# Kernel optimization log

Hardware: AMD Instinct MI355X
Metric: run time of the kernel (lower is better)

## Reference

```python
import jax, jax.numpy as jnp
import numpy as np

BN_EPS = 1e-5
LN_EPS = 1e-5


def setup_inputs() -> dict:
    key = jax.random.key(0)
    ks = jax.random.split(key, 8)
    B, D, T = 16, 96, 512  # batch, enc_in (channels), d_model (time/feature)
    H = 2 * T
    residual = jax.random.normal(ks[0], (B, D, T), dtype=jnp.float32)
    # BatchNorm1d(enc_in) affine params
    bn_gamma = jnp.ones((D,), dtype=jnp.float32)
    bn_beta = jnp.zeros((D,), dtype=jnp.float32)
    # LayerNorm(d_model) affine params
    ln_gamma = jnp.ones((T,), dtype=jnp.float32)
    ln_beta = jnp.zeros((T,), dtype=jnp.float32)
    # MLP: Linear(T, 2T) -> GELU -> Linear(2T, T)
    W1 = jax.random.normal(ks[1], (T, H), dtype=jnp.float32) / np.float32(np.sqrt(T))
    b1 = jnp.zeros((H,), dtype=jnp.float32)
    W2 = jax.random.normal(ks[2], (H, T), dtype=jnp.float32) / np.float32(np.sqrt(H))
    b2 = jnp.zeros((T,), dtype=jnp.float32)
    return {"residual": residual, "bn_gamma": bn_gamma, "bn_beta": bn_beta,
            "ln_gamma": ln_gamma, "ln_beta": ln_beta,
            "W1": W1, "b1": b1, "W2": W2, "b2": b2}


def _var_cor_attention(x):
    # x: [B, D, T]; queries = keys = values = x
    B, D, T = x.shape
    f = jnp.fft.rfft(x, axis=-1)                       # [B, D, F]
    # pairwise spectral product q_i * conj(k_j): [B, D, D, F]
    res = f[:, :, None, :] * jnp.conj(f[:, None, :, :])
    corr = jnp.fft.irfft(res, axis=-1).mean(axis=-1)   # [B, D, D]
    scale = np.float32(1.0 / np.sqrt(T))
    corr = jax.nn.softmax(corr * scale, axis=-1)
    V = jnp.einsum('bsd,bde->bse', corr, x)            # [B, D, T]
    return V


def reference(residual, bn_gamma, bn_beta, ln_gamma, ln_beta, W1, b1, W2, b2):
    # attention + residual
    x = _var_cor_attention(residual) + residual        # [B, D, T]
    # BatchNorm1d over channel dim D: stats over (B, T), biased variance
    mu = x.mean(axis=(0, 2), keepdims=True)
    var = ((x - mu) ** 2).mean(axis=(0, 2), keepdims=True)
    x = (x - mu) * jax.lax.rsqrt(var + BN_EPS)
    x = x * bn_gamma[None, :, None] + bn_beta[None, :, None]
    # MLP (exact GELU, torch default) + residual
    h = jax.nn.gelu(jnp.einsum('bdt,th->bdh', x, W1) + b1, approximate=False)
    y = jnp.einsum('bdh,ht->bdt', h, W2) + b2 + x
    # LayerNorm over last dim T
    mu2 = y.mean(axis=-1, keepdims=True)
    var2 = ((y - mu2) ** 2).mean(axis=-1, keepdims=True)
    y = (y - mu2) * jax.lax.rsqrt(var2 + LN_EPS)
    return y * ln_gamma + ln_beta
```

## Files before the change

kernel.cpp:

```cpp
#include <hip/hip_runtime.h>
#include <math.h>
#include <stdint.h>

#define BB 16
#define DD 96
#define TT 512
#define HH 1024
#define NROW (BB*DD)

typedef __attribute__((ext_vector_type(4))) float floatx4;
typedef __attribute__((ext_vector_type(8))) short short8;

#define WSOFF_X     0
#define WSOFF_HFRAG 0
#define WSOFF_XROW  (3*1024*1024)
#define WSOFF_XFRAG (WSOFF_XROW + NROW*TT*2)
#define WSOFF_W1BF  (WSOFF_XFRAG + NROW*TT*2)
#define WSOFF_W2BF  (WSOFF_W1BF + TT*HH*2)
#define WSOFF_A     (WSOFF_W2BF + HH*TT*2)
#define WSOFF_P1    (WSOFF_A + BB*DD*DD*4)
#define WSOFF_P2    (WSOFF_P1 + DD*128*4)

__device__ __forceinline__ uint16_t f2bf(float v) {
    uint32_t u = __float_as_uint(v);
    uint32_t r = 0x7fffu + ((u >> 16) & 1u);
    return (uint16_t)((u + r) >> 16);
}
__device__ __forceinline__ float bf2f(uint16_t v) {
    return __uint_as_float(((uint32_t)v) << 16);
}

#define KT1 (TT/32)
#define KT2 (HH/32)
__device__ __forceinline__ size_t afrag1_slot(int row, int k) {
    return ((size_t)((row >> 4)*KT1 + (k >> 5))*64 + ((k >> 3) & 3)*16 + (row & 15));
}

__global__ __launch_bounds__(256) void k_prep(const float* __restrict__ r,
                                              float* __restrict__ A) {
    __shared__ float sl[DD];
    int b = blockIdx.x;
    int tid = threadIdx.x;
    int w = tid >> 6, lane = tid & 63;
    for (int rr = 0; rr < 24; ++rr) {
        int i = w*24 + rr;
        const float* p = r + ((size_t)b*DD + i)*TT;
        float acc = 0.f;
        #pragma unroll
        for (int s = 0; s < TT/64; ++s) acc += p[lane + s*64];
        #pragma unroll
        for (int o = 32; o > 0; o >>= 1) acc += __shfl_down(acc, o, 64);
        if (lane == 0) sl[i] = acc;
    }
    __syncthreads();
    int i = tid;
    if (i < DD) {
        const float c = 1.0f / (512.0f * 22.627416997969522f);
        float si = sl[i] * c;
        float m = -1e30f;
        for (int j = 0; j < DD; ++j) m = fmaxf(m, si * sl[j]);
        float sum = 0.f;
        for (int j = 0; j < DD; ++j) sum += expf(si * sl[j] - m);
        float inv = 1.0f / sum;
        float* Ao = A + ((size_t)b*DD + i)*DD;
        for (int j = 0; j < DD; ++j) Ao[j] = expf(si * sl[j] - m) * inv;
    }
}

__global__ __launch_bounds__(256) void k_attw(const float* __restrict__ r,
                                              const float* __restrict__ A,
                                              const float* __restrict__ W1,
                                              const float* __restrict__ W2,
                                              float* __restrict__ x,
                                              uint16_t* __restrict__ w1bf,
                                              uint16_t* __restrict__ w2bf,
                                              float* __restrict__ P1,
                                              float* __restrict__ P2) {
    int bx = blockIdx.x;
    int tid = threadIdx.x;
    int w = tid >> 6, lane = tid & 63;
    if (bx < 512) {
        int blk = bx*4 + w;
        int q = lane >> 4, l15 = lane & 15;
        const float* W; uint16_t* out; int KT, N, b;
        if (blk < 1024) { W = W1; out = w1bf; KT = 16; N = 1024; b = blk; }
        else            { W = W2; out = w2bf; KT = 32; N = 512;  b = blk - 1024; }
        int tile_n = b / KT, tile_k = b % KT;
        const float* src = W + (size_t)(tile_k*32 + q*8)*N + tile_n*16 + l15;
        uint16_t tmp[8];
        #pragma unroll
        for (int j = 0; j < 8; ++j) tmp[j] = f2bf(src[(size_t)j*N]);
        uint16_t* dst = out + ((size_t)b*64 + lane)*8;
        *reinterpret_cast<ushort4*>(dst)     = *reinterpret_cast<ushort4*>(&tmp[0]);
        *reinterpret_cast<ushort4*>(dst + 4) = *reinterpret_cast<ushort4*>(&tmp[4]);
        return;
    }
    __shared__ float rlds[DD*64];
    int idx = bx - 512;
    int b = idx & 15, chunk = (idx >> 4) & 7, ig = idx >> 7;
    int t0 = chunk * 64;
    const float4* rb4 = reinterpret_cast<const float4*>(r + (size_t)b*DD*TT);
    float4* rl4 = reinterpret_cast<float4*>(rlds);
    #pragma unroll
    for (int s = 0; s < 6; ++s) {
        int ii = tid + s*256;
        rl4[ii] = rb4[(size_t)(ii >> 4)*(TT/4) + (t0 >> 2) + (ii & 15)];
    }
    __syncthreads();
    int wu = __builtin_amdgcn_readfirstlane(w);
    int i0 = ig*24 + wu*6;
    const float* Ab = A + ((size_t)b*DD + i0)*DD;
    float acc[6];
    #pragma unroll
    for (int rr = 0; rr < 6; ++rr) acc[rr] = rlds[(i0+rr)*64 + lane];
    #pragma unroll 4
    for (int j4 = 0; j4 < DD/4; ++j4) {
        float4 a[6];
        #pragma unroll
        for (int rr = 0; rr < 6; ++rr)
            a[rr] = *reinterpret_cast<const float4*>(Ab + rr*DD + j4*4);
        float rv[4];
        #pragma unroll
        for (int u = 0; u < 4; ++u) rv[u] = rlds[(j4*4+u)*64 + lane];
        #pragma unroll
        for (int rr = 0; rr < 6; ++rr) {
            acc[rr] = fmaf(a[rr].x, rv[0], acc[rr]);
            acc[rr] = fmaf(a[rr].y, rv[1], acc[rr]);
            acc[rr] = fmaf(a[rr].z, rv[2], acc[rr]);
            acc[rr] = fmaf(a[rr].w, rv[3], acc[rr]);
        }
    }
    int p = b*8 + chunk;
    #pragma unroll
    for (int rr = 0; rr < 6; ++rr) {
        int i = i0 + rr;
        x[((size_t)b*DD + i)*TT + t0 + lane] = acc[rr];
        float ls = acc[rr], ls2 = acc[rr]*acc[rr];
        #pragma unroll
        for (int o = 32; o > 0; o >>= 1) {
            ls  += __shfl_down(ls,  o, 64);
            ls2 += __shfl_down(ls2, o, 64);
        }
        if (lane == 0) { P1[i*128 + p] = ls; P2[i*128 + p] = ls2; }
    }
}

__global__ __launch_bounds__(256) void k_bnx(const float* __restrict__ x,
                                             const float* __restrict__ P1,
                                             const float* __restrict__ P2,
                                             const float* __restrict__ g,
                                             const float* __restrict__ bt,
                                             uint16_t* __restrict__ xrow,
                                             uint16_t* __restrict__ xfrag) {
    __shared__ float rr1[4], rr2[4], scsh[4];
    int blk = blockIdx.x;
    int tid = threadIdx.x;
    int wid = tid >> 6, lane = tid & 63;
    int r0 = blk*2;
    int d0 = r0 % DD, d1 = (r0+1) % DD;
    int d = (wid < 2) ? d0 : d1;
    int p = (wid & 1)*64 + lane;
    float v1 = P1[d*128 + p], v2 = P2[d*128 + p];
    #pragma unroll
    for (int o = 32; o > 0; o >>= 1) {
        v1 += __shfl_down(v1, o, 64);
        v2 += __shfl_down(v2, o, 64);
    }
    if (lane == 0) { rr1[wid] = v1; rr2[wid] = v2; }
    __syncthreads();
    if (tid < 2) {
        float s1 = rr1[tid*2] + rr1[tid*2+1];
        float s2 = rr2[tid*2] + rr2[tid*2+1];
        const float invn = 1.0f / (float)(BB*TT);
        float mu  = s1 * invn;
        float var = s2 * invn - mu*mu;
        float rs  = rsqrtf(var + 1e-5f);
        int dd = (tid == 0) ? d0 : d1;
        float scale = rs * g[dd];
        scsh[tid*2]   = scale;
        scsh[tid*2+1] = bt[dd] - mu*scale;
    }
    __syncthreads();
    int half = tid >> 7;
    int row = r0 + half;
    int k0 = (tid & 127) * 4;
    float scd = scsh[half*2], shd = scsh[half*2+1];
    float4 v = *reinterpret_cast<const float4*>(&x[(size_t)row*TT + k0]);
    ushort4 o;
    o.x = f2bf(v.x*scd + shd);
    o.y = f2bf(v.y*scd + shd);
    o.z = f2bf(v.z*scd + shd);
    o.w = f2bf(v.w*scd + shd);
    *reinterpret_cast<ushort4*>(&xrow[(size_t)row*TT + k0]) = o;
    size_t slot = afrag1_slot(row, k0);
    *reinterpret_cast<ushort4*>(&xfrag[slot*8 + (k0 & 7)]) = o;
}

__global__ __launch_bounds__(256) void k_gemm1(const uint16_t* __restrict__ xfrag,
                                               const uint16_t* __restrict__ w1bf,
                                               const float* __restrict__ b1,
                                               uint16_t* __restrict__ hfrag) {
    __shared__ __align__(16) uint16_t cs[16][136];
    int tid = threadIdx.x;
    int wave = tid >> 6, lane = tid & 63;
    int q = lane >> 4, l15 = lane & 15;
    int mtile = blockIdx.x;
    int n0 = blockIdx.y * 128 + wave * 32;
    floatx4 acc[2] = {};
    const uint16_t* ap  = xfrag + ((size_t)mtile*KT1*64 + lane)*8;
    const uint16_t* b0p = w1bf + ((size_t)((n0>>4)    )*16*64 + lane)*8;
    const uint16_t* b1p = w1bf + ((size_t)((n0>>4) + 1)*16*64 + lane)*8;
    #pragma unroll
    for (int kk = 0; kk < 16; ++kk) {
        short8 a  = *reinterpret_cast<const short8*>(ap  + kk*512);
        short8 b0 = *reinterpret_cast<const short8*>(b0p + kk*512);
        short8 b1 = *reinterpret_cast<const short8*>(b1p + kk*512);
        acc[0] = __builtin_amdgcn_mfma_f32_16x16x32_bf16(a, b0, acc[0], 0, 0, 0);
        acc[1] = __builtin_amdgcn_mfma_f32_16x16x32_bf16(a, b1, acc[1], 0, 0, 0);
    }
    #pragma unroll
    for (int nf = 0; nf < 2; ++nf) {
        int coll = wave*32 + nf*16 + l15;
        float bias = b1[blockIdx.y*128 + coll];
        #pragma unroll
        for (int r = 0; r < 4; ++r) {
            float v = acc[nf][r] + bias;
            float gl = 0.5f * v * (1.0f + erff(v * 0.7071067811865475f));
            cs[q*4 + r][coll] = f2bf(gl);
        }
    }
    __syncthreads();
    int c = wave;
    const uint4* src = reinterpret_cast<const uint4*>(&cs[l15][c*32 + q*8]);
    size_t chunk = (size_t)mtile*KT2 + (blockIdx.y*4 + c);
    reinterpret_cast<uint4*>(hfrag)[chunk*64 + lane] = *src;
}

__global__ __launch_bounds__(256) void k_gemm2(const uint16_t* __restrict__ hfrag,
                                               const uint16_t* __restrict__ w2bf,
                                               const float* __restrict__ b2,
                                               const uint16_t* __restrict__ xrow,
                                               float* __restrict__ y) {
    int tid = threadIdx.x;
    int wave = tid >> 6, lane = tid & 63;
    int q = lane >> 4, l15 = lane & 15;
    int mtile = blockIdx.x;
    int m0 = mtile * 16;
    int n0 = blockIdx.y * 128 + wave * 32;
    floatx4 acc[2] = {};
    const uint16_t* ap  = hfrag + ((size_t)mtile*KT2*64 + lane)*8;
    const uint16_t* b0p = w2bf + ((size_t)((n0>>4)    )*32*64 + lane)*8;
    const uint16_t* b1p = w2bf + ((size_t)((n0>>4) + 1)*32*64 + lane)*8;
    #pragma unroll
    for (int kk = 0; kk < 32; ++kk) {
        short8 a  = *reinterpret_cast<const short8*>(ap  + kk*512);
        short8 b0 = *reinterpret_cast<const short8*>(b0p + kk*512);
        short8 b1 = *reinterpret_cast<const short8*>(b1p + kk*512);
        acc[0] = __builtin_amdgcn_mfma_f32_16x16x32_bf16(a, b0, acc[0], 0, 0, 0);
        acc[1] = __builtin_amdgcn_mfma_f32_16x16x32_bf16(a, b1, acc[1], 0, 0, 0);
    }
    #pragma unroll
    for (int nf = 0; nf < 2; ++nf) {
        int col = n0 + nf*16 + l15;
        float bias = b2[col];
        #pragma unroll
        for (int r = 0; r < 4; ++r) {
            int row = m0 + q*4 + r;
            float xb = bf2f(xrow[(size_t)row*TT + col]);
            y[(size_t)row*TT + col] = acc[nf][r] + bias + xb;
        }
    }
}

__global__ __launch_bounds__(64) void k_ln(float* __restrict__ y,
                                           const float* __restrict__ lng,
                                           const float* __restrict__ lnb) {
    int row = blockIdx.x;
    int lane = threadIdx.x;
    float4* p = reinterpret_cast<float4*>(y + (size_t)row*TT);
    float4 v0 = p[lane*2], v1 = p[lane*2 + 1];
    float s  = v0.x+v0.y+v0.z+v0.w + v1.x+v1.y+v1.z+v1.w;
    float s2 = v0.x*v0.x+v0.y*v0.y+v0.z*v0.z+v0.w*v0.w
             + v1.x*v1.x+v1.y*v1.y+v1.z*v1.z+v1.w*v1.w;
    #pragma unroll
    for (int o = 1; o < 64; o <<= 1) {
        s  += __shfl_xor(s,  o, 64);
        s2 += __shfl_xor(s2, o, 64);
    }
    float mu = s * (1.0f/TT);
    float var = s2 * (1.0f/TT) - mu*mu;
    float rs = rsqrtf(var + 1e-5f);
    const float4* g4 = reinterpret_cast<const float4*>(lng);
    const float4* b4 = reinterpret_cast<const float4*>(lnb);
    float4 g0 = g4[lane*2], g1 = g4[lane*2+1];
    float4 bb0 = b4[lane*2], bb1 = b4[lane*2+1];
    float4 o0, o1;
    o0.x = (v0.x-mu)*rs*g0.x + bb0.x;  o0.y = (v0.y-mu)*rs*g0.y + bb0.y;
    o0.z = (v0.z-mu)*rs*g0.z + bb0.z;  o0.w = (v0.w-mu)*rs*g0.w + bb0.w;
    o1.x = (v1.x-mu)*rs*g1.x + bb1.x;  o1.y = (v1.y-mu)*rs*g1.y + bb1.y;
    o1.z = (v1.z-mu)*rs*g1.z + bb1.z;  o1.w = (v1.w-mu)*rs*g1.w + bb1.w;
    p[lane*2] = o0;  p[lane*2+1] = o1;
}

extern "C" void kernel_launch(void* const* d_in, const int* in_sizes, int n_in,
                              void* d_out, int out_size, void* d_ws, size_t ws_size,
                              hipStream_t stream) {
    (void)in_sizes; (void)n_in; (void)out_size; (void)ws_size;
    const float* residual = (const float*)d_in[0];
    const float* bng = (const float*)d_in[1];
    const float* bnb = (const float*)d_in[2];
    const float* lng = (const float*)d_in[3];
    const float* lnb = (const float*)d_in[4];
    const float* W1  = (const float*)d_in[5];
    const float* b1  = (const float*)d_in[6];
    const float* W2  = (const float*)d_in[7];
    const float* b2  = (const float*)d_in[8];
    float* out = (float*)d_out;
    char* ws = (char*)d_ws;
    float*    x     = (float*)(ws + WSOFF_X);
    uint16_t* hfrag = (uint16_t*)(ws + WSOFF_HFRAG);
    uint16_t* xrow  = (uint16_t*)(ws + WSOFF_XROW);
    uint16_t* xfrag = (uint16_t*)(ws + WSOFF_XFRAG);
    uint16_t* w1bf  = (uint16_t*)(ws + WSOFF_W1BF);
    uint16_t* w2bf  = (uint16_t*)(ws + WSOFF_W2BF);
    float*    A     = (float*)(ws + WSOFF_A);
    float*    P1    = (float*)(ws + WSOFF_P1);
    float*    P2    = (float*)(ws + WSOFF_P2);

    k_prep<<<BB, 256, 0, stream>>>(residual, A);
    k_attw<<<1024, 256, 0, stream>>>(residual, A, W1, W2, x, w1bf, w2bf, P1, P2);
    k_bnx<<<NROW/2, 256, 0, stream>>>(x, P1, P2, bng, bnb, xrow, xfrag);
    k_gemm1<<<dim3(96, 8), 256, 0, stream>>>(xfrag, w1bf, b1, hfrag);
    k_gemm2<<<dim3(96, 4), 256, 0, stream>>>(hfrag, w2bf, b2, xrow, out);
    k_ln<<<NROW, 64, 0, stream>>>(out, lng, lnb);
}
```

Measured before the change: 127.9 us.

## Fuse all stages into one cooperative persistent kernel with grid syncs

Replaces the six separate kernel launches with a single cooperative kernel of 512 blocks that runs each stage in turn, separated by grid-wide barriers. It also parallelises the row sums and softmax of the attention weights across many blocks, where the old prep kernel used only 16 blocks. The aim is to remove launch gaps and the serial prep bottleneck. In exchange it adds grid.sync costs, caps the grid at 512 blocks with stage loops, and falls back to seven ordinary launches if the cooperative launch fails.

```diff
diff --git a/kernel.cpp b/kernel.cpp
--- a/kernel.cpp
+++ b/kernel.cpp
@@ -1,6 +1,9 @@
 #include <hip/hip_runtime.h>
+#include <hip/hip_cooperative_groups.h>
 #include <math.h>
 #include <stdint.h>
+
+namespace cg = cooperative_groups;
 
 #define BB 16
 #define DD 96
@@ -12,7 +15,6 @@
 typedef __attribute__((ext_vector_type(8))) short short8;
 
 #define WSOFF_X     0
-#define WSOFF_HFRAG 0
 #define WSOFF_XROW  (3*1024*1024)
 #define WSOFF_XFRAG (WSOFF_XROW + NROW*TT*2)
 #define WSOFF_W1BF  (WSOFF_XFRAG + NROW*TT*2)
@@ -20,6 +22,7 @@
 #define WSOFF_A     (WSOFF_W2BF + HH*TT*2)
 #define WSOFF_P1    (WSOFF_A + BB*DD*DD*4)
 #define WSOFF_P2    (WSOFF_P1 + DD*128*4)
+#define WSOFF_S     (WSOFF_P2 + DD*128*4)
 
 __device__ __forceinline__ uint16_t f2bf(float v) {
     uint32_t u = __float_as_uint(v);
@@ -36,270 +39,278 @@
     return ((size_t)((row >> 4)*KT1 + (k >> 5))*64 + ((k >> 3) & 3)*16 + (row & 15));
 }
 
-__global__ __launch_bounds__(256) void k_prep(const float* __restrict__ r,
-                                              float* __restrict__ A) {
-    __shared__ float sl[DD];
-    int b = blockIdx.x;
-    int tid = threadIdx.x;
-    int w = tid >> 6, lane = tid & 63;
-    for (int rr = 0; rr < 24; ++rr) {
-        int i = w*24 + rr;
-        const float* p = r + ((size_t)b*DD + i)*TT;
-        float acc = 0.f;
-        #pragma unroll
-        for (int s = 0; s < TT/64; ++s) acc += p[lane + s*64];
-        #pragma unroll
-        for (int o = 32; o > 0; o >>= 1) acc += __shfl_down(acc, o, 64);
-        if (lane == 0) sl[i] = acc;
-    }
-    __syncthreads();
-    int i = tid;
-    if (i < DD) {
-        const float c = 1.0f / (512.0f * 22.627416997969522f);
-        float si = sl[i] * c;
-        float m = -1e30f;
-        for (int j = 0; j < DD; ++j) m = fmaxf(m, si * sl[j]);
-        float sum = 0.f;
-        for (int j = 0; j < DD; ++j) sum += expf(si * sl[j] - m);
-        float inv = 1.0f / sum;
-        float* Ao = A + ((size_t)b*DD + i)*DD;
-        for (int j = 0; j < DD; ++j) Ao[j] = expf(si * sl[j] - m) * inv;
-    }
-}
-
-__global__ __launch_bounds__(256) void k_attw(const float* __restrict__ r,
-                                              const float* __restrict__ A,
-                                              const float* __restrict__ W1,
-                                              const float* __restrict__ W2,
-                                              float* __restrict__ x,
-                                              uint16_t* __restrict__ w1bf,
-                                              uint16_t* __restrict__ w2bf,
-                                              float* __restrict__ P1,
-                                              float* __restrict__ P2) {
+__global__ __launch_bounds__(256, 4) void k_fused(
+        int plo, int phi, int coop,
+        const float* __restrict__ r,
+        const float* __restrict__ bng, const float* __restrict__ bnb,
+        const float* __restrict__ lng, const float* __restrict__ lnb,
+        const float* __restrict__ W1,  const float* __restrict__ b1,
+        const float* __restrict__ W2,  const float* __restrict__ b2,
+        float* __restrict__ out,
+        float* __restrict__ x, uint16_t* __restrict__ xrow,
+        uint16_t* __restrict__ xfrag, uint16_t* __restrict__ w1bf,
+        uint16_t* __restrict__ w2bf, float* __restrict__ A,
+        float* __restrict__ P1, float* __restrict__ P2,
+        float* __restrict__ s) {
+    cg::grid_group grid = cg::this_grid();
+    __shared__ __align__(16) float sbuf[DD*64];
+    uint16_t* hfrag = reinterpret_cast<uint16_t*>(x);
     int bx = blockIdx.x;
     int tid = threadIdx.x;
     int w = tid >> 6, lane = tid & 63;
-    if (bx < 512) {
-        int blk = bx*4 + w;
-        int q = lane >> 4, l15 = lane & 15;
-        const float* W; uint16_t* out; int KT, N, b;
-        if (blk < 1024) { W = W1; out = w1bf; KT = 16; N = 1024; b = blk; }
-        else            { W = W2; out = w2bf; KT = 32; N = 512;  b = blk - 1024; }
-        int tile_n = b / KT, tile_k = b % KT;
-        const float* src = W + (size_t)(tile_k*32 + q*8)*N + tile_n*16 + l15;
-        uint16_t tmp[8];
+    int q = lane >> 4, l15 = lane & 15;
+
+    if (plo <= 0 && 0 <= phi) {
         #pragma unroll
-        for (int j = 0; j < 8; ++j) tmp[j] = f2bf(src[(size_t)j*N]);
-        uint16_t* dst = out + ((size_t)b*64 + lane)*8;
-        *reinterpret_cast<ushort4*>(dst)     = *reinterpret_cast<ushort4*>(&tmp[0]);
-        *reinterpret_cast<ushort4*>(dst + 4) = *reinterpret_cast<ushort4*>(&tmp[4]);
-        return;
-    }
-    __shared__ float rlds[DD*64];
-    int idx = bx - 512;
-    int b = idx & 15, chunk = (idx >> 4) & 7, ig = idx >> 7;
-    int t0 = chunk * 64;
-    const float4* rb4 = reinterpret_cast<const float4*>(r + (size_t)b*DD*TT);
-    float4* rl4 = reinterpret_cast<float4*>(rlds);
-    #pragma unroll
-    for (int s = 0; s < 6; ++s) {
-        int ii = tid + s*256;
-        rl4[ii] = rb4[(size_t)(ii >> 4)*(TT/4) + (t0 >> 2) + (ii & 15)];
-    }
-    __syncthreads();
-    int wu = __builtin_amdgcn_readfirstlane(w);
-    int i0 = ig*24 + wu*6;
-    const float* Ab = A + ((size_t)b*DD + i0)*DD;
-    float acc[6];
-    #pragma unroll
-    for (int rr = 0; rr < 6; ++rr) acc[rr] = rlds[(i0+rr)*64 + lane];
-    #pragma unroll 4
-    for (int j4 = 0; j4 < DD/4; ++j4) {
-        float4 a[6];
-        #pragma unroll
-        for (int rr = 0; rr < 6; ++rr)
-            a[rr] = *reinterpret_cast<const float4*>(Ab + rr*DD + j4*4);
-        float rv[4];
-        #pragma unroll
-        for (int u = 0; u < 4; ++u) rv[u] = rlds[(j4*4+u)*64 + lane];
-        #pragma unroll
-        for (int rr = 0; rr < 6; ++rr) {
-            acc[rr] = fmaf(a[rr].x, rv[0], acc[rr]);
-            acc[rr] = fmaf(a[rr].y, rv[1], acc[rr]);
-            acc[rr] = fmaf(a[rr].z, rv[2], acc[rr]);
-            acc[rr] = fmaf(a[rr].w, rv[3], acc[rr]);
-        }
-    }
-    int p = b*8 + chunk;
-    #pragma unroll
-    for (int rr = 0; rr < 6; ++rr) {
-        int i = i0 + rr;
-        x[((size_t)b*DD + i)*TT + t0 + lane] = acc[rr];
-        float ls = acc[rr], ls2 = acc[rr]*acc[rr];
-        #pragma unroll
-        for (int o = 32; o > 0; o >>= 1) {
-            ls  += __shfl_down(ls,  o, 64);
-            ls2 += __shfl_down(ls2, o, 64);
-        }
-        if (lane == 0) { P1[i*128 + p] = ls; P2[i*128 + p] = ls2; }
-    }
-}
-
-__global__ __launch_bounds__(256) void k_bnx(const float* __restrict__ x,
-                                             const float* __restrict__ P1,
-                                             const float* __restrict__ P2,
-                                             const float* __restrict__ g,
-                                             const float* __restrict__ bt,
-                                             uint16_t* __restrict__ xrow,
-                                             uint16_t* __restrict__ xfrag) {
-    __shared__ float rr1[4], rr2[4], scsh[4];
-    int blk = blockIdx.x;
-    int tid = threadIdx.x;
-    int wid = tid >> 6, lane = tid & 63;
-    int r0 = blk*2;
-    int d0 = r0 % DD, d1 = (r0+1) % DD;
-    int d = (wid < 2) ? d0 : d1;
-    int p = (wid & 1)*64 + lane;
-    float v1 = P1[d*128 + p], v2 = P2[d*128 + p];
-    #pragma unroll
-    for (int o = 32; o > 0; o >>= 1) {
-        v1 += __shfl_down(v1, o, 64);
-        v2 += __shfl_down(v2, o, 64);
-    }
-    if (lane == 0) { rr1[wid] = v1; rr2[wid] = v2; }
-    __syncthreads();
-    if (tid < 2) {
-        float s1 = rr1[tid*2] + rr1[tid*2+1];
-        float s2 = rr2[tid*2] + rr2[tid*2+1];
-        const float invn = 1.0f / (float)(BB*TT);
-        float mu  = s1 * invn;
-        float var = s2 * invn - mu*mu;
-        float rs  = rsqrtf(var + 1e-5f);
-        int dd = (tid == 0) ? d0 : d1;
-        float scale = rs * g[dd];
-        scsh[tid*2]   = scale;
-        scsh[tid*2+1] = bt[dd] - mu*scale;
-    }
-    __syncthreads();
-    int half = tid >> 7;
-    int row = r0 + half;
-    int k0 = (tid & 127) * 4;
-    float scd = scsh[half*2], shd = scsh[half*2+1];
-    float4 v = *reinterpret_cast<const float4*>(&x[(size_t)row*TT + k0]);
-    ushort4 o;
-    o.x = f2bf(v.x*scd + shd);
-    o.y = f2bf(v.y*scd + shd);
-    o.z = f2bf(v.z*scd + shd);
-    o.w = f2bf(v.w*scd + shd);
-    *reinterpret_cast<ushort4*>(&xrow[(size_t)row*TT + k0]) = o;
-    size_t slot = afrag1_slot(row, k0);
-    *reinterpret_cast<ushort4*>(&xfrag[slot*8 + (k0 & 7)]) = o;
-}
-
-__global__ __launch_bounds__(256) void k_gemm1(const uint16_t* __restrict__ xfrag,
-                                               const uint16_t* __restrict__ w1bf,
-                                               const float* __restrict__ b1,
-                                               uint16_t* __restrict__ hfrag) {
-    __shared__ __align__(16) uint16_t cs[16][136];
-    int tid = threadIdx.x;
-    int wave = tid >> 6, lane = tid & 63;
-    int q = lane >> 4, l15 = lane & 15;
-    int mtile = blockIdx.x;
-    int n0 = blockIdx.y * 128 + wave * 32;
-    floatx4 acc[2] = {};
-    const uint16_t* ap  = xfrag + ((size_t)mtile*KT1*64 + lane)*8;
-    const uint16_t* b0p = w1bf + ((size_t)((n0>>4)    )*16*64 + lane)*8;
-    const uint16_t* b1p = w1bf + ((size_t)((n0>>4) + 1)*16*64 + lane)*8;
-    #pragma unroll
-    for (int kk = 0; kk < 16; ++kk) {
-        short8 a  = *reinterpret_cast<const short8*>(ap  + kk*512);
-        short8 b0 = *reinterpret_cast<const short8*>(b0p + kk*512);
-        short8 b1 = *reinterpret_cast<const short8*>(b1p + kk*512);
-        acc[0] = __builtin_amdgcn_mfma_f32_16x16x32_bf16(a, b0, acc[0], 0, 0, 0);
-        acc[1] = __builtin_amdgcn_mfma_f32_16x16x32_bf16(a, b1, acc[1], 0, 0, 0);
-    }
-    #pragma unroll
-    for (int nf = 0; nf < 2; ++nf) {
-        int coll = wave*32 + nf*16 + l15;
-        float bias = b1[blockIdx.y*128 + coll];
-        #pragma unroll
-        for (int r = 0; r < 4; ++r) {
-            float v = acc[nf][r] + bias;
-            float gl = 0.5f * v * (1.0f + erff(v * 0.7071067811865475f));
-            cs[q*4 + r][coll] = f2bf(gl);
-        }
-    }
-    __syncthreads();
-    int c = wave;
-    const uint4* src = reinterpret_cast<const uint4*>(&cs[l15][c*32 + q*8]);
-    size_t chunk = (size_t)mtile*KT2 + (blockIdx.y*4 + c);
-    reinterpret_cast<uint4*>(hfrag)[chunk*64 + lane] = *src;
-}
-
-__global__ __launch_bounds__(256) void k_gemm2(const uint16_t* __restrict__ hfrag,
-                                               const uint16_t* __restrict__ w2bf,
-                                               const float* __restrict__ b2,
-                                               const uint16_t* __restrict__ xrow,
-                                               float* __restrict__ y) {
-    int tid = threadIdx.x;
-    int wave = tid >> 6, lane = tid & 63;
-    int q = lane >> 4, l15 = lane & 15;
-    int mtile = blockIdx.x;
-    int m0 = mtile * 16;
-    int n0 = blockIdx.y * 128 + wave * 32;
-    floatx4 acc[2] = {};
-    const uint16_t* ap  = hfrag + ((size_t)mtile*KT2*64 + lane)*8;
-    const uint16_t* b0p = w2bf + ((size_t)((n0>>4)    )*32*64 + lane)*8;
-    const uint16_t* b1p = w2bf + ((size_t)((n0>>4) + 1)*32*64 + lane)*8;
-    #pragma unroll
-    for (int kk = 0; kk < 32; ++kk) {
-        short8 a  = *reinterpret_cast<const short8*>(ap  + kk*512);
-        short8 b0 = *reinterpret_cast<const short8*>(b0p + kk*512);
-        short8 b1 = *reinterpret_cast<const short8*>(b1p + kk*512);
-        acc[0] = __builtin_amdgcn_mfma_f32_16x16x32_bf16(a, b0, acc[0], 0, 0, 0);
-        acc[1] = __builtin_amdgcn_mfma_f32_16x16x32_bf16(a, b1, acc[1], 0, 0, 0);
-    }
-    #pragma unroll
-    for (int nf = 0; nf < 2; ++nf) {
-        int col = n0 + nf*16 + l15;
-        float bias = b2[col];
-        #pragma unroll
-        for (int r = 0; r < 4; ++r) {
-            int row = m0 + q*4 + r;
-            float xb = bf2f(xrow[(size_t)row*TT + col]);
-            y[(size_t)row*TT + col] = acc[nf][r] + bias + xb;
-        }
-    }
-}
-
-__global__ __launch_bounds__(64) void k_ln(float* __restrict__ y,
-                                           const float* __restrict__ lng,
-                                           const float* __restrict__ lnb) {
-    int row = blockIdx.x;
-    int lane = threadIdx.x;
-    float4* p = reinterpret_cast<float4*>(y + (size_t)row*TT);
-    float4 v0 = p[lane*2], v1 = p[lane*2 + 1];
-    float s  = v0.x+v0.y+v0.z+v0.w + v1.x+v1.y+v1.z+v1.w;
-    float s2 = v0.x*v0.x+v0.y*v0.y+v0.z*v0.z+v0.w*v0.w
-             + v1.x*v1.x+v1.y*v1.y+v1.z*v1.z+v1.w*v1.w;
-    #pragma unroll
-    for (int o = 1; o < 64; o <<= 1) {
-        s  += __shfl_xor(s,  o, 64);
-        s2 += __shfl_xor(s2, o, 64);
-    }
-    float mu = s * (1.0f/TT);
-    float var = s2 * (1.0f/TT) - mu*mu;
-    float rs = rsqrtf(var + 1e-5f);
-    const float4* g4 = reinterpret_cast<const float4*>(lng);
-    const float4* b4 = reinterpret_cast<const float4*>(lnb);
-    float4 g0 = g4[lane*2], g1 = g4[lane*2+1];
-    float4 bb0 = b4[lane*2], bb1 = b4[lane*2+1];
-    float4 o0, o1;
-    o0.x = (v0.x-mu)*rs*g0.x + bb0.x;  o0.y = (v0.y-mu)*rs*g0.y + bb0.y;
-    o0.z = (v0.z-mu)*rs*g0.z + bb0.z;  o0.w = (v0.w-mu)*rs*g0.w + bb0.w;
-    o1.x = (v1.x-mu)*rs*g1.x + bb1.x;  o1.y = (v1.y-mu)*rs*g1.y + bb1.y;
-    o1.z = (v1.z-mu)*rs*g1.z + bb1.z;  o1.w = (v1.w-mu)*rs*g1.w + bb1.w;
-    p[lane*2] = o0;  p[lane*2+1] = o1;
+        for (int p = 0; p < 3; ++p) {
+            int row = bx + 512*p;
+            float2 v = reinterpret_cast<const float2*>(r + (size_t)row*TT)[tid];
+            float acc = v.x + v.y;
+            #pragma unroll
+            for (int o = 32; o > 0; o >>= 1) acc += __shfl_down(acc, o, 64);
+            if (lane == 0) sbuf[w] = acc;
+            __syncthreads();
+            if (tid == 0) s[row] = sbuf[0]+sbuf[1]+sbuf[2]+sbuf[3];
+            __syncthreads();
+        }
+    }
+    if (coop) grid.sync();
+
+    if (plo <= 1 && 1 <= phi) {
+        int gw = bx*4 + w;
+        if (gw < NROW) {
+            int b = gw / DD, i = gw - b*DD;
+            const float* sb = s + b*DD;
+            const float c = 1.0f / (512.0f * 22.627416997969522f);
+            float si = sb[i] * c;
+            float v0 = si * sb[lane];
+            float v1 = (lane < DD-64) ? si * sb[64 + lane] : -1e30f;
+            float m = fmaxf(v0, v1);
+            #pragma unroll
+            for (int o = 32; o > 0; o >>= 1) m = fmaxf(m, __shfl_xor(m, o, 64));
+            float e0 = expf(v0 - m);
+            float e1 = (lane < DD-64) ? expf(v1 - m) : 0.f;
+            float sum = e0 + e1;
+            #pragma unroll
+            for (int o = 32; o > 0; o >>= 1) sum += __shfl_xor(sum, o, 64);
+            float inv = 1.0f / sum;
+            float* Ao = A + (size_t)gw*DD;
+            Ao[lane] = e0 * inv;
+            if (lane < DD-64) Ao[64 + lane] = e1 * inv;
+        }
+    }
+    if (coop) grid.sync();
+
+    if (plo <= 2 && 2 <= phi) {
+        {
+            int blk = bx*4 + w;
+            const float* W; uint16_t* outw; int KT, N, b;
+            if (blk < 1024) { W = W1; outw = w1bf; KT = 16; N = 1024; b = blk; }
+            else            { W = W2; outw = w2bf; KT = 32; N = 512;  b = blk - 1024; }
+            int tile_n = b / KT, tile_k = b % KT;
+            const float* src = W + (size_t)(tile_k*32 + q*8)*N + tile_n*16 + l15;
+            uint16_t tmp[8];
+            #pragma unroll
+            for (int j = 0; j < 8; ++j) tmp[j] = f2bf(src[(size_t)j*N]);
+            uint16_t* dst = outw + ((size_t)b*64 + lane)*8;
+            *reinterpret_cast<ushort4*>(dst)     = *reinterpret_cast<ushort4*>(&tmp[0]);
+            *reinterpret_cast<ushort4*>(dst + 4) = *reinterpret_cast<ushort4*>(&tmp[4]);
+        }
+        {
+            int b = bx & 15, chunk = (bx >> 4) & 7, ig = bx >> 7;
+            int t0 = chunk * 64;
+            const float4* rb4 = reinterpret_cast<const float4*>(r + (size_t)b*DD*TT);
+            float4* rl4 = reinterpret_cast<float4*>(sbuf);
+            #pragma unroll
+            for (int ss = 0; ss < 6; ++ss) {
+                int ii = tid + ss*256;
+                rl4[ii] = rb4[(size_t)(ii >> 4)*(TT/4) + (t0 >> 2) + (ii & 15)];
+            }
+            __syncthreads();
+            int wu = __builtin_amdgcn_readfirstlane(w);
+            int i0 = ig*24 + wu*6;
+            const float* Ab = A + ((size_t)b*DD + i0)*DD;
+            float acc[6];
+            #pragma unroll
+            for (int rr = 0; rr < 6; ++rr) acc[rr] = sbuf[(i0+rr)*64 + lane];
+            #pragma unroll 4
+            for (int j4 = 0; j4 < DD/4; ++j4) {
+                float4 a[6];
+                #pragma unroll
+                for (int rr = 0; rr < 6; ++rr)
+                    a[rr] = *reinterpret_cast<const float4*>(Ab + rr*DD + j4*4);
+                float rv[4];
+                #pragma unroll
+                for (int u = 0; u < 4; ++u) rv[u] = sbuf[(j4*4+u)*64 + lane];
+                #pragma unroll
+                for (int rr = 0; rr < 6; ++rr) {
+                    acc[rr] = fmaf(a[rr].x, rv[0], acc[rr]);
+                    acc[rr] = fmaf(a[rr].y, rv[1], acc[rr]);
+                    acc[rr] = fmaf(a[rr].z, rv[2], acc[rr]);
+                    acc[rr] = fmaf(a[rr].w, rv[3], acc[rr]);
+                }
+            }
+            int p = b*8 + chunk;
+            #pragma unroll
+            for (int rr = 0; rr < 6; ++rr) {
+                int i = i0 + rr;
+                x[((size_t)b*DD + i)*TT + t0 + lane] = acc[rr];
+                float ls = acc[rr], ls2 = acc[rr]*acc[rr];
+                #pragma unroll
+                for (int o = 32; o > 0; o >>= 1) {
+                    ls  += __shfl_down(ls,  o, 64);
+                    ls2 += __shfl_down(ls2, o, 64);
+                }
+                if (lane == 0) { P1[i*128 + p] = ls; P2[i*128 + p] = ls2; }
+            }
+            __syncthreads();
+        }
+    }
+    if (coop) grid.sync();
+
+    if (plo <= 3 && 3 <= phi) {
+        for (int u = bx; u < 768; u += 512) {
+            float* rr1 = sbuf; float* rr2 = sbuf + 4; float* scsh = sbuf + 8;
+            int r0 = u*2;
+            int d0 = r0 % DD, d1 = (r0+1) % DD;
+            int d = (w < 2) ? d0 : d1;
+            int p = (w & 1)*64 + lane;
+            float v1 = P1[d*128 + p], v2 = P2[d*128 + p];
+            #pragma unroll
+            for (int o = 32; o > 0; o >>= 1) {
+                v1 += __shfl_down(v1, o, 64);
+                v2 += __shfl_down(v2, o, 64);
+            }
+            if (lane == 0) { rr1[w] = v1; rr2[w] = v2; }
+            __syncthreads();
+            if (tid < 2) {
+                float s1 = rr1[tid*2] + rr1[tid*2+1];
+                float s2 = rr2[tid*2] + rr2[tid*2+1];
+                const float invn = 1.0f / (float)(BB*TT);
+                float mu  = s1 * invn;
+                float var = s2 * invn - mu*mu;
+                float rs  = rsqrtf(var + 1e-5f);
+                int dd = (tid == 0) ? d0 : d1;
+                float scale = rs * bng[dd];
+                scsh[tid*2]   = scale;
+                scsh[tid*2+1] = bnb[dd] - mu*scale;
+            }
+            __syncthreads();
+            int half = tid >> 7;
+            int row = r0 + half;
+            int k0 = (tid & 127) * 4;
+            float scd = scsh[half*2], shd = scsh[half*2+1];
+            float4 v = *reinterpret_cast<const float4*>(&x[(size_t)row*TT + k0]);
+            ushort4 o;
+            o.x = f2bf(v.x*scd + shd);
+            o.y = f2bf(v.y*scd + shd);
+            o.z = f2bf(v.z*scd + shd);
+            o.w = f2bf(v.w*scd + shd);
+            *reinterpret_cast<ushort4*>(&xrow[(size_t)row*TT + k0]) = o;
+            size_t slot = afrag1_slot(row, k0);
+            *reinterpret_cast<ushort4*>(&xfrag[slot*8 + (k0 & 7)]) = o;
+            __syncthreads();
+        }
+    }
+    if (coop) grid.sync();
+
+    if (plo <= 4 && 4 <= phi) {
+        for (int u = bx; u < 768; u += 512) {
+            uint16_t* cs = reinterpret_cast<uint16_t*>(sbuf);
+            int mtile = u >> 3, ny = u & 7;
+            int n0 = ny * 128 + w * 32;
+            floatx4 acc[2] = {};
+            const uint16_t* ap  = xfrag + ((size_t)mtile*KT1*64 + lane)*8;
+            const uint16_t* b0p = w1bf + ((size_t)((n0>>4)    )*16*64 + lane)*8;
+            const uint16_t* b1p = w1bf + ((size_t)((n0>>4) + 1)*16*64 + lane)*8;
+            #pragma unroll
+            for (int kk = 0; kk < 16; ++kk) {
+                short8 a  = *reinterpret_cast<const short8*>(ap  + kk*512);
+                short8 b0 = *reinterpret_cast<const short8*>(b0p + kk*512);
+                short8 b1 = *reinterpret_cast<const short8*>(b1p + kk*512);
+                acc[0] = __builtin_amdgcn_mfma_f32_16x16x32_bf16(a, b0, acc[0], 0, 0, 0);
+                acc[1] = __builtin_amdgcn_mfma_f32_16x16x32_bf16(a, b1, acc[1], 0, 0, 0);
+            }
+            #pragma unroll
+            for (int nf = 0; nf < 2; ++nf) {
+                int coll = w*32 + nf*16 + l15;
+                float bias = b1[ny*128 + coll];
+                #pragma unroll
+                for (int rr = 0; rr < 4; ++rr) {
+                    float v = acc[nf][rr] + bias;
+                    float gl = 0.5f * v * (1.0f + erff(v * 0.7071067811865475f));
+                    cs[(q*4 + rr)*136 + coll] = f2bf(gl);
+                }
+            }
+            __syncthreads();
+            const uint4* src = reinterpret_cast<const uint4*>(&cs[l15*136 + w*32 + q*8]);
+            size_t chunk = (size_t)mtile*KT2 + (ny*4 + w);
+            reinterpret_cast<uint4*>(hfrag)[chunk*64 + lane] = *src;
+            __syncthreads();
+        }
+    }
+    if (coop) grid.sync();
+
+    if (plo <= 5 && 5 <= phi) {
+        if (bx < 384) {
+            int mtile = bx >> 2, ny = bx & 3;
+            int m0 = mtile * 16;
+            int n0 = ny * 128 + w * 32;
+            floatx4 acc[2] = {};
+            const uint16_t* ap  = hfrag + ((size_t)mtile*KT2*64 + lane)*8;
+            const uint16_t* b0p = w2bf + ((size_t)((n0>>4)    )*32*64 + lane)*8;
+            const uint16_t* b1p = w2bf + ((size_t)((n0>>4) + 1)*32*64 + lane)*8;
+            #pragma unroll
+            for (int kk = 0; kk < 32; ++kk) {
+                short8 a  = *reinterpret_cast<const short8*>(ap  + kk*512);
+                short8 b0 = *reinterpret_cast<const short8*>(b0p + kk*512);
+                short8 b1 = *reinterpret_cast<const short8*>(b1p + kk*512);
+                acc[0] = __builtin_amdgcn_mfma_f32_16x16x32_bf16(a, b0, acc[0], 0, 0, 0);
+                acc[1] = __builtin_amdgcn_mfma_f32_16x16x32_bf16(a, b1, acc[1], 0, 0, 0);
+            }
+            #pragma unroll
+            for (int nf = 0; nf < 2; ++nf) {
+                int col = n0 + nf*16 + l15;
+                float bias = b2[col];
+                #pragma unroll
+                for (int rr = 0; rr < 4; ++rr) {
+                    int row = m0 + q*4 + rr;
+                    float xb = bf2f(xrow[(size_t)row*TT + col]);
+                    out[(size_t)row*TT + col] = acc[nf][rr] + bias + xb;
+                }
+            }
+        }
+    }
+    if (coop) grid.sync();
+
+    if (plo <= 6 && 6 <= phi) {
+        int gw = bx*4 + w;
+        if (gw < NROW) {
+            float4* p = reinterpret_cast<float4*>(out + (size_t)gw*TT);
+            float4 v0 = p[lane*2], v1 = p[lane*2 + 1];
+            float sa = v0.x+v0.y+v0.z+v0.w + v1.x+v1.y+v1.z+v1.w;
+            float s2 = v0.x*v0.x+v0.y*v0.y+v0.z*v0.z+v0.w*v0.w
+                     + v1.x*v1.x+v1.y*v1.y+v1.z*v1.z+v1.w*v1.w;
+            #pragma unroll
+            for (int o = 1; o < 64; o <<= 1) {
+                sa += __shfl_xor(sa, o, 64);
+                s2 += __shfl_xor(s2, o, 64);
+            }
+            float mu = sa * (1.0f/TT);
+            float var = s2 * (1.0f/TT) - mu*mu;
+            float rs = rsqrtf(var + 1e-5f);
+            const float4* g4 = reinterpret_cast<const float4*>(lng);
+            const float4* b4 = reinterpret_cast<const float4*>(lnb);
+            float4 g0 = g4[lane*2], g1 = g4[lane*2+1];
+            float4 bb0 = b4[lane*2], bb1 = b4[lane*2+1];
+            float4 o0, o1;
+            o0.x = (v0.x-mu)*rs*g0.x + bb0.x;  o0.y = (v0.y-mu)*rs*g0.y + bb0.y;
+            o0.z = (v0.z-mu)*rs*g0.z + bb0.z;  o0.w = (v0.w-mu)*rs*g0.w + bb0.w;
+            o1.x = (v1.x-mu)*rs*g1.x + bb1.x;  o1.y = (v1.y-mu)*rs*g1.y + bb1.y;
+            o1.z = (v1.z-mu)*rs*g1.z + bb1.z;  o1.w = (v1.w-mu)*rs*g1.w + bb1.w;
+            p[lane*2] = o0;  p[lane*2+1] = o1;
+        }
+    }
 }
 
 extern "C" void kernel_launch(void* const* d_in, const int* in_sizes, int n_in,
@@ -318,7 +329,6 @@
     float* out = (float*)d_out;
     char* ws = (char*)d_ws;
     float*    x     = (float*)(ws + WSOFF_X);
-    uint16_t* hfrag = (uint16_t*)(ws + WSOFF_HFRAG);
     uint16_t* xrow  = (uint16_t*)(ws + WSOFF_XROW);
     uint16_t* xfrag = (uint16_t*)(ws + WSOFF_XFRAG);
     uint16_t* w1bf  = (uint16_t*)(ws + WSOFF_W1BF);
@@ -326,11 +336,22 @@
     float*    A     = (float*)(ws + WSOFF_A);
     float*    P1    = (float*)(ws + WSOFF_P1);
     float*    P2    = (float*)(ws + WSOFF_P2);
-
-    k_prep<<<BB, 256, 0, stream>>>(residual, A);
-    k_attw<<<1024, 256, 0, stream>>>(residual, A, W1, W2, x, w1bf, w2bf, P1, P2);
-    k_bnx<<<NROW/2, 256, 0, stream>>>(x, P1, P2, bng, bnb, xrow, xfrag);
-    k_gemm1<<<dim3(96, 8), 256, 0, stream>>>(xfrag, w1bf, b1, hfrag);
-    k_gemm2<<<dim3(96, 4), 256, 0, stream>>>(hfrag, w2bf, b2, xrow, out);
-    k_ln<<<NROW, 64, 0, stream>>>(out, lng, lnb);
-}
+    float*    s     = (float*)(ws + WSOFF_S);
+
+    int plo = 0, phi = 6, coop = 1;
+    void* args[] = { (void*)&plo, (void*)&phi, (void*)&coop,
+                     (void*)&residual, (void*)&bng, (void*)&bnb, (void*)&lng,
+                     (void*)&lnb, (void*)&W1, (void*)&b1, (void*)&W2, (void*)&b2,
+                     (void*)&out, (void*)&x, (void*)&xrow, (void*)&xfrag,
+                     (void*)&w1bf, (void*)&w2bf, (void*)&A, (void*)&P1,
+                     (void*)&P2, (void*)&s };
+    hipError_t rc = hipLaunchCooperativeKernel((const void*)k_fused, dim3(512),
+                                               dim3(256), args, 0, stream);
+    if (rc != hipSuccess) {
+        for (int p = 0; p < 7; ++p) {
+            k_fused<<<512, 256, 0, stream>>>(p, p, 0,
+                residual, bng, bnb, lng, lnb, W1, b1, W2, b2, out,
+                x, xrow, xfrag, w1bf, w2bf, A, P1, P2, s);
+        }
+    }
+}
```

Result: slower. 439.1 us (+243.3%).

## Parallelize row sums, fuse softmax into attention, fuse LayerNorm into GEMM2 tail

Applied to the files above, without the earlier changes.

Replaces the 16-block prep kernel, which computed row sums and a materialized softmax matrix, with a 512-block row-sum kernel. Each attention block now recomputes its 24 softmax rows from the row sums in shared memory, so the global A matrix is no longer written and read. LayerNorm is folded into GEMM2: the last of the four column-tile blocks per row tile, detected with an atomic counter plus thread fences, normalizes those rows, and the separate LN launch goes away. The cost is redundant softmax work across attention blocks and a serialized LN tail in the last-arriving block.

```diff
diff --git a/kernel.cpp b/kernel.cpp
--- a/kernel.cpp
+++ b/kernel.cpp
@@ -12,14 +12,14 @@
 typedef __attribute__((ext_vector_type(8))) short short8;
 
 #define WSOFF_X     0
-#define WSOFF_HFRAG 0
 #define WSOFF_XROW  (3*1024*1024)
 #define WSOFF_XFRAG (WSOFF_XROW + NROW*TT*2)
 #define WSOFF_W1BF  (WSOFF_XFRAG + NROW*TT*2)
 #define WSOFF_W2BF  (WSOFF_W1BF + TT*HH*2)
-#define WSOFF_A     (WSOFF_W2BF + HH*TT*2)
-#define WSOFF_P1    (WSOFF_A + BB*DD*DD*4)
+#define WSOFF_P1    (WSOFF_W2BF + HH*TT*2)
 #define WSOFF_P2    (WSOFF_P1 + DD*128*4)
+#define WSOFF_S     (WSOFF_P2 + DD*128*4)
+#define WSOFF_CNT   (WSOFF_S + NROW*4)
 
 __device__ __forceinline__ uint16_t f2bf(float v) {
     uint32_t u = __float_as_uint(v);
@@ -36,39 +36,29 @@
     return ((size_t)((row >> 4)*KT1 + (k >> 5))*64 + ((k >> 3) & 3)*16 + (row & 15));
 }
 
-__global__ __launch_bounds__(256) void k_prep(const float* __restrict__ r,
-                                              float* __restrict__ A) {
-    __shared__ float sl[DD];
-    int b = blockIdx.x;
-    int tid = threadIdx.x;
+__global__ __launch_bounds__(256) void k_rowsum(const float* __restrict__ r,
+                                                float* __restrict__ s,
+                                                int* __restrict__ cnt) {
+    __shared__ float sbuf[4];
+    int bx = blockIdx.x, tid = threadIdx.x;
     int w = tid >> 6, lane = tid & 63;
-    for (int rr = 0; rr < 24; ++rr) {
-        int i = w*24 + rr;
-        const float* p = r + ((size_t)b*DD + i)*TT;
-        float acc = 0.f;
-        #pragma unroll
-        for (int s = 0; s < TT/64; ++s) acc += p[lane + s*64];
+    if (bx == 0 && tid < DD) cnt[tid] = 0;
+    #pragma unroll
+    for (int p = 0; p < 3; ++p) {
+        int row = bx + 512*p;
+        float2 v = reinterpret_cast<const float2*>(r + (size_t)row*TT)[tid];
+        float acc = v.x + v.y;
         #pragma unroll
         for (int o = 32; o > 0; o >>= 1) acc += __shfl_down(acc, o, 64);
-        if (lane == 0) sl[i] = acc;
-    }
-    __syncthreads();
-    int i = tid;
-    if (i < DD) {
-        const float c = 1.0f / (512.0f * 22.627416997969522f);
-        float si = sl[i] * c;
-        float m = -1e30f;
-        for (int j = 0; j < DD; ++j) m = fmaxf(m, si * sl[j]);
-        float sum = 0.f;
-        for (int j = 0; j < DD; ++j) sum += expf(si * sl[j] - m);
-        float inv = 1.0f / sum;
-        float* Ao = A + ((size_t)b*DD + i)*DD;
-        for (int j = 0; j < DD; ++j) Ao[j] = expf(si * sl[j] - m) * inv;
+        if (lane == 0) sbuf[w] = acc;
+        __syncthreads();
+        if (tid == 0) s[row] = sbuf[0]+sbuf[1]+sbuf[2]+sbuf[3];
+        __syncthreads();
     }
 }
 
 __global__ __launch_bounds__(256) void k_attw(const float* __restrict__ r,
-                                              const float* __restrict__ A,
+                                              const float* __restrict__ s,
                                               const float* __restrict__ W1,
                                               const float* __restrict__ W2,
                                               float* __restrict__ x,
@@ -76,40 +66,63 @@
                                               uint16_t* __restrict__ w2bf,
                                               float* __restrict__ P1,
                                               float* __restrict__ P2) {
-    int bx = blockIdx.x;
-    int tid = threadIdx.x;
+    __shared__ __align__(16) float rlds[DD*64];
+    __shared__ float sls[DD];
+    __shared__ __align__(16) float Atile[24][DD];
+    int bx = blockIdx.x, tid = threadIdx.x;
     int w = tid >> 6, lane = tid & 63;
+    int q = lane >> 4, l15 = lane & 15;
     if (bx < 512) {
         int blk = bx*4 + w;
-        int q = lane >> 4, l15 = lane & 15;
-        const float* W; uint16_t* out; int KT, N, b;
-        if (blk < 1024) { W = W1; out = w1bf; KT = 16; N = 1024; b = blk; }
-        else            { W = W2; out = w2bf; KT = 32; N = 512;  b = blk - 1024; }
+        const float* W; uint16_t* outw; int KT, N, b;
+        if (blk < 1024) { W = W1; outw = w1bf; KT = 16; N = 1024; b = blk; }
+        else            { W = W2; outw = w2bf; KT = 32; N = 512;  b = blk - 1024; }
         int tile_n = b / KT, tile_k = b % KT;
         const float* src = W + (size_t)(tile_k*32 + q*8)*N + tile_n*16 + l15;
         uint16_t tmp[8];
         #pragma unroll
         for (int j = 0; j < 8; ++j) tmp[j] = f2bf(src[(size_t)j*N]);
-        uint16_t* dst = out + ((size_t)b*64 + lane)*8;
+        uint16_t* dst = outw + ((size_t)b*64 + lane)*8;
         *reinterpret_cast<ushort4*>(dst)     = *reinterpret_cast<ushort4*>(&tmp[0]);
         *reinterpret_cast<ushort4*>(dst + 4) = *reinterpret_cast<ushort4*>(&tmp[4]);
         return;
     }
-    __shared__ float rlds[DD*64];
     int idx = bx - 512;
     int b = idx & 15, chunk = (idx >> 4) & 7, ig = idx >> 7;
     int t0 = chunk * 64;
     const float4* rb4 = reinterpret_cast<const float4*>(r + (size_t)b*DD*TT);
     float4* rl4 = reinterpret_cast<float4*>(rlds);
     #pragma unroll
-    for (int s = 0; s < 6; ++s) {
-        int ii = tid + s*256;
+    for (int ss = 0; ss < 6; ++ss) {
+        int ii = tid + ss*256;
         rl4[ii] = rb4[(size_t)(ii >> 4)*(TT/4) + (t0 >> 2) + (ii & 15)];
     }
-    __syncthreads();
+    if (tid < DD) sls[tid] = s[b*DD + tid];
+    __syncthreads();
+
     int wu = __builtin_amdgcn_readfirstlane(w);
     int i0 = ig*24 + wu*6;
-    const float* Ab = A + ((size_t)b*DD + i0)*DD;
+    const float c = 1.0f / (512.0f * 22.627416997969522f);
+    float sl0 = sls[lane];
+    float sl1 = (lane < DD-64) ? sls[64 + lane] : 0.f;
+    #pragma unroll
+    for (int rr = 0; rr < 6; ++rr) {
+        float si = sls[i0+rr] * c;
+        float v0 = si * sl0;
+        float v1 = (lane < DD-64) ? si * sl1 : -1e30f;
+        float m = fmaxf(v0, v1);
+        #pragma unroll
+        for (int o = 32; o > 0; o >>= 1) m = fmaxf(m, __shfl_xor(m, o, 64));
+        float e0 = expf(v0 - m);
+        float e1 = (lane < DD-64) ? expf(v1 - m) : 0.f;
+        float sum = e0 + e1;
+        #pragma unroll
+        for (int o = 32; o > 0; o >>= 1) sum += __shfl_xor(sum, o, 64);
+        float inv = 1.0f / sum;
+        Atile[wu*6 + rr][lane] = e0 * inv;
+        if (lane < DD-64) Atile[wu*6 + rr][64 + lane] = e1 * inv;
+    }
+
     float acc[6];
     #pragma unroll
     for (int rr = 0; rr < 6; ++rr) acc[rr] = rlds[(i0+rr)*64 + lane];
@@ -118,7 +131,7 @@
         float4 a[6];
         #pragma unroll
         for (int rr = 0; rr < 6; ++rr)
-            a[rr] = *reinterpret_cast<const float4*>(Ab + rr*DD + j4*4);
+            a[rr] = *reinterpret_cast<const float4*>(&Atile[wu*6 + rr][j4*4]);
         float rv[4];
         #pragma unroll
         for (int u = 0; u < 4; ++u) rv[u] = rlds[(j4*4+u)*64 + lane];
@@ -153,8 +166,7 @@
                                              uint16_t* __restrict__ xrow,
                                              uint16_t* __restrict__ xfrag) {
     __shared__ float rr1[4], rr2[4], scsh[4];
-    int blk = blockIdx.x;
-    int tid = threadIdx.x;
+    int blk = blockIdx.x, tid = threadIdx.x;
     int wid = tid >> 6, lane = tid & 63;
     int r0 = blk*2;
     int d0 = r0 % DD, d1 = (r0+1) % DD;
@@ -236,11 +248,15 @@
     reinterpret_cast<uint4*>(hfrag)[chunk*64 + lane] = *src;
 }
 
-__global__ __launch_bounds__(256) void k_gemm2(const uint16_t* __restrict__ hfrag,
-                                               const uint16_t* __restrict__ w2bf,
-                                               const float* __restrict__ b2,
-                                               const uint16_t* __restrict__ xrow,
-                                               float* __restrict__ y) {
+__global__ __launch_bounds__(256) void k_gemm2ln(const uint16_t* __restrict__ hfrag,
+                                                 const uint16_t* __restrict__ w2bf,
+                                                 const float* __restrict__ b2,
+                                                 const uint16_t* __restrict__ xrow,
+                                                 const float* __restrict__ lng,
+                                                 const float* __restrict__ lnb,
+                                                 int* __restrict__ cnt,
+                                                 float* __restrict__ y) {
+    __shared__ int last;
     int tid = threadIdx.x;
     int wave = tid >> 6, lane = tid & 63;
     int q = lane >> 4, l15 = lane & 15;
@@ -270,36 +286,38 @@
             y[(size_t)row*TT + col] = acc[nf][r] + bias + xb;
         }
     }
-}
-
-__global__ __launch_bounds__(64) void k_ln(float* __restrict__ y,
-                                           const float* __restrict__ lng,
-                                           const float* __restrict__ lnb) {
-    int row = blockIdx.x;
-    int lane = threadIdx.x;
-    float4* p = reinterpret_cast<float4*>(y + (size_t)row*TT);
-    float4 v0 = p[lane*2], v1 = p[lane*2 + 1];
-    float s  = v0.x+v0.y+v0.z+v0.w + v1.x+v1.y+v1.z+v1.w;
-    float s2 = v0.x*v0.x+v0.y*v0.y+v0.z*v0.z+v0.w*v0.w
-             + v1.x*v1.x+v1.y*v1.y+v1.z*v1.z+v1.w*v1.w;
-    #pragma unroll
-    for (int o = 1; o < 64; o <<= 1) {
-        s  += __shfl_xor(s,  o, 64);
-        s2 += __shfl_xor(s2, o, 64);
-    }
-    float mu = s * (1.0f/TT);
-    float var = s2 * (1.0f/TT) - mu*mu;
-    float rs = rsqrtf(var + 1e-5f);
-    const float4* g4 = reinterpret_cast<const float4*>(lng);
-    const float4* b4 = reinterpret_cast<const float4*>(lnb);
-    float4 g0 = g4[lane*2], g1 = g4[lane*2+1];
-    float4 bb0 = b4[lane*2], bb1 = b4[lane*2+1];
-    float4 o0, o1;
-    o0.x = (v0.x-mu)*rs*g0.x + bb0.x;  o0.y = (v0.y-mu)*rs*g0.y + bb0.y;
-    o0.z = (v0.z-mu)*rs*g0.z + bb0.z;  o0.w = (v0.w-mu)*rs*g0.w + bb0.w;
-    o1.x = (v1.x-mu)*rs*g1.x + bb1.x;  o1.y = (v1.y-mu)*rs*g1.y + bb1.y;
-    o1.z = (v1.z-mu)*rs*g1.z + bb1.z;  o1.w = (v1.w-mu)*rs*g1.w + bb1.w;
-    p[lane*2] = o0;  p[lane*2+1] = o1;
+    __threadfence();
+    if (tid == 0) last = atomicAdd(&cnt[mtile], 1);
+    __syncthreads();
+    if (last != 3) return;
+    __threadfence();
+    #pragma unroll
+    for (int rl = 0; rl < 4; ++rl) {
+        int row = m0 + wave*4 + rl;
+        float4* p = reinterpret_cast<float4*>(y + (size_t)row*TT);
+        float4 v0 = p[lane*2], v1 = p[lane*2 + 1];
+        float sa = v0.x+v0.y+v0.z+v0.w + v1.x+v1.y+v1.z+v1.w;
+        float s2 = v0.x*v0.x+v0.y*v0.y+v0.z*v0.z+v0.w*v0.w
+                 + v1.x*v1.x+v1.y*v1.y+v1.z*v1.z+v1.w*v1.w;
+        #pragma unroll
+        for (int o = 1; o < 64; o <<= 1) {
+            sa += __shfl_xor(sa, o, 64);
+            s2 += __shfl_xor(s2, o, 64);
+        }
+        float mu = sa * (1.0f/TT);
+        float var = s2 * (1.0f/TT) - mu*mu;
+        float rs = rsqrtf(var + 1e-5f);
+        const float4* g4 = reinterpret_cast<const float4*>(lng);
+        const float4* b4 = reinterpret_cast<const float4*>(lnb);
+        float4 g0 = g4[lane*2], g1 = g4[lane*2+1];
+        float4 bb0 = b4[lane*2], bb1 = b4[lane*2+1];
+        float4 o0, o1;
+        o0.x = (v0.x-mu)*rs*g0.x + bb0.x;  o0.y = (v0.y-mu)*rs*g0.y + bb0.y;
+        o0.z = (v0.z-mu)*rs*g0.z + bb0.z;  o0.w = (v0.w-mu)*rs*g0.w + bb0.w;
+        o1.x = (v1.x-mu)*rs*g1.x + bb1.x;  o1.y = (v1.y-mu)*rs*g1.y + bb1.y;
+        o1.z = (v1.z-mu)*rs*g1.z + bb1.z;  o1.w = (v1.w-mu)*rs*g1.w + bb1.w;
+        p[lane*2] = o0;  p[lane*2+1] = o1;
+    }
 }
 
 extern "C" void kernel_launch(void* const* d_in, const int* in_sizes, int n_in,
@@ -318,19 +336,19 @@
     float* out = (float*)d_out;
     char* ws = (char*)d_ws;
     float*    x     = (float*)(ws + WSOFF_X);
-    uint16_t* hfrag = (uint16_t*)(ws + WSOFF_HFRAG);
+    uint16_t* hfrag = (uint16_t*)(ws + WSOFF_X);
     uint16_t* xrow  = (uint16_t*)(ws + WSOFF_XROW);
     uint16_t* xfrag = (uint16_t*)(ws + WSOFF_XFRAG);
     uint16_t* w1bf  = (uint16_t*)(ws + WSOFF_W1BF);
     uint16_t* w2bf  = (uint16_t*)(ws + WSOFF_W2BF);
-    float*    A     = (float*)(ws + WSOFF_A);
     float*    P1    = (float*)(ws + WSOFF_P1);
     float*    P2    = (float*)(ws + WSOFF_P2);
-
-    k_prep<<<BB, 256, 0, stream>>>(residual, A);
-    k_attw<<<1024, 256, 0, stream>>>(residual, A, W1, W2, x, w1bf, w2bf, P1, P2);
+    float*    s     = (float*)(ws + WSOFF_S);
+    int*      cnt   = (int*)(ws + WSOFF_CNT);
+
+    k_rowsum<<<512, 256, 0, stream>>>(residual, s, cnt);
+    k_attw<<<1024, 256, 0, stream>>>(residual, s, W1, W2, x, w1bf, w2bf, P1, P2);
     k_bnx<<<NROW/2, 256, 0, stream>>>(x, P1, P2, bng, bnb, xrow, xfrag);
     k_gemm1<<<dim3(96, 8), 256, 0, stream>>>(xfrag, w1bf, b1, hfrag);
-    k_gemm2<<<dim3(96, 4), 256, 0, stream>>>(hfrag, w2bf, b2, xrow, out);
-    k_ln<<<NROW, 64, 0, stream>>>(out, lng, lnb);
-}
+    k_gemm2ln<<<dim3(96, 4), 256, 0, stream>>>(hfrag, w2bf, b2, xrow, lng, lnb, cnt, out);
+}
```

Result: slower. 161.9 us (+26.6%).
